# Performance work log

Hardware: AMD Instinct MI355X
Metric: run time of the kernel (lower is better)

## Reference

```python
import jax, jax.numpy as jnp
import numpy as np

B, S, DIM = 64, 576, 768
KEEP_TOKEN = 64  # module keeps KEEP_TOKEN-1 top patches + 1 pooled extra token
HID = 128       # autoencoder bottleneck


def setup_inputs() -> dict:
    key = jax.random.key(0)
    k1, k2, k3, k4 = jax.random.split(key, 4)
    cls_emb = jax.random.normal(k1, (B, DIM), dtype=jnp.float32)
    fm = jax.random.normal(k2, (B, S, DIM), dtype=jnp.float32)
    # autoencoder: Linear(dim,128) -> Tanh -> Linear(128,dim); y = x @ W + b
    W1 = jax.random.normal(k3, (DIM, HID), dtype=jnp.float32) / np.sqrt(DIM)
    b1 = jnp.zeros((HID,), dtype=jnp.float32)
    W2 = jax.random.normal(k4, (HID, DIM), dtype=jnp.float32) / np.sqrt(HID)
    b2 = jnp.zeros((DIM,), dtype=jnp.float32)
    return {"cls_emb": cls_emb, "fm": fm, "W1": W1, "b1": b1, "W2": W2, "b2": b2}


def reference(cls_emb, fm, W1, b1, W2, b2):
    # cls attention scores over patch tokens: [B, S]
    cls_attn = jnp.einsum('bd,bsd->bs', cls_emb, fm)
    # top-(K-1) patches by cls attention (largest, sorted)
    _, idx = jax.lax.top_k(cls_attn, KEEP_TOKEN - 1)           # [B, K-1]
    top_token = jnp.take_along_axis(fm, idx[:, :, None], axis=1)  # [B, K-1, DIM]
    # mask selected positions (one_hot(idx).sum(1) -> 0/1 since topk idx unique)
    batch_ix = jnp.arange(fm.shape[0])[:, None]
    one_hot_idx = jnp.zeros_like(cls_attn).at[batch_ix, idx].add(1.0)  # [B, S]
    weight = jax.nn.softmax(one_hot_idx * -10000.0 + cls_attn, axis=1)[:, :, None]
    extra_token = jnp.sum(weight * fm, axis=1, keepdims=True)  # [B, 1, DIM]
    visual_tokens = jnp.concatenate([top_token, extra_token], axis=1)  # [B, K, DIM]
    ae = lambda x: jnp.tanh(x @ W1 + b1) @ W2 + b2
    return ae(visual_tokens), ae(cls_emb)
```

## Files before the change

### kernel.cpp

```cpp
#include <hip/hip_runtime.h>
#include <math.h>

#define BB   64
#define SS   576
#define DD   768
#define KTOP 63
#define KEEP 64
#define HH   128
#define NROW (BB*KEEP + BB)
#define SCH  24

typedef unsigned long long ull;

__global__ __launch_bounds__(256) void k_scores(const float* __restrict__ cls,
                                                const float* __restrict__ fm,
                                                float* __restrict__ scores)
{
  int gw = (blockIdx.x * blockDim.x + threadIdx.x) >> 6;
  int lane = threadIdx.x & 63;
  if (gw >= BB * SS) return;
  int b = gw / SS, s = gw - b * SS;
  const float4* frow = (const float4*)(fm + ((size_t)b * SS + s) * DD);
  const float4* crow = (const float4*)(cls + (size_t)b * DD);
  double acc = 0.0;
#pragma unroll
  for (int j = 0; j < 3; ++j) {
    float4 f = frow[lane + 64 * j];
    float4 c = crow[lane + 64 * j];
    acc += (double)f.x * c.x + (double)f.y * c.y + (double)f.z * c.z + (double)f.w * c.w;
  }
#pragma unroll
  for (int off = 32; off > 0; off >>= 1) acc += __shfl_down(acc, off, 64);
  if (lane == 0) scores[(size_t)b * SS + s] = (float)acc;
}

__global__ __launch_bounds__(576) void k_rank(const float* __restrict__ scores,
                                              int* __restrict__ idxout,
                                              float* __restrict__ wprime)
{
  __shared__ ull keys[SS];
  __shared__ float redm[9], redz[9];
  int b = blockIdx.x, tid = threadIdx.x;
  int lane = tid & 63, wid = tid >> 6;
  float sc = scores[(size_t)b * SS + tid];
  unsigned int u = __float_as_uint(sc);
  u = (u & 0x80000000u) ? ~u : (u | 0x80000000u);
  ull key = ((ull)u << 32) | (ull)(0xFFFFFFFFu - (unsigned)tid);
  keys[tid] = key;
  __syncthreads();
  int rank = 0;
#pragma unroll 8
  for (int s = 0; s < SS; ++s) rank += (keys[s] > key) ? 1 : 0;
  bool sel = rank < KTOP;
  if (sel) idxout[b * KEEP + rank] = tid;
  float m = sel ? -1e30f : sc;
#pragma unroll
  for (int off = 32; off; off >>= 1) m = fmaxf(m, __shfl_xor(m, off, 64));
  if (lane == 0) redm[wid] = m;
  __syncthreads();
  float M = redm[0];
#pragma unroll
  for (int i = 1; i < 9; ++i) M = fmaxf(M, redm[i]);
  float e = sel ? 0.f : expf(sc - M);
  float z = e;
#pragma unroll
  for (int off = 32; off; off >>= 1) z += __shfl_xor(z, off, 64);
  if (lane == 0) redz[wid] = z;
  __syncthreads();
  float Z = redz[0];
#pragma unroll
  for (int i = 1; i < 9; ++i) Z += redz[i];
  wprime[(size_t)b * SS + tid] = e / Z;
}

__global__ __launch_bounds__(192) void k_extra2(const float* __restrict__ wprime,
                                                const float* __restrict__ fm,
                                                float* __restrict__ epart)
{
  int b = blockIdx.x, p = blockIdx.y, tid = threadIdx.x;
  const float* fbase = fm + ((size_t)b * SS + p * SCH) * DD + tid * 4;
  const float* wp = wprime + (size_t)b * SS + p * SCH;
  float4 acc = make_float4(0.f, 0.f, 0.f, 0.f);
#pragma unroll
  for (int r = 0; r < SCH; ++r) {
    float w = wp[r];
    float4 v = *(const float4*)(fbase + (size_t)r * DD);
    acc.x = fmaf(w, v.x, acc.x); acc.y = fmaf(w, v.y, acc.y);
    acc.z = fmaf(w, v.z, acc.z); acc.w = fmaf(w, v.w, acc.w);
  }
  *(float4*)(epart + ((size_t)(b * SCH + p) * DD) + tid * 4) = acc;
}

__global__ __launch_bounds__(256) void k_ered(const float* __restrict__ epart,
                                              float* __restrict__ extra)
{
  int i = blockIdx.x * 256 + threadIdx.x;
  int b = i / (DD / 4), c4 = i - b * (DD / 4);
  const float4* P = (const float4*)epart;
  float4 s = make_float4(0.f, 0.f, 0.f, 0.f);
#pragma unroll
  for (int p = 0; p < SCH; ++p) {
    float4 t = P[(size_t)(b * SCH + p) * (DD / 4) + c4];
    s.x += t.x; s.y += t.y; s.z += t.z; s.w += t.w;
  }
  ((float4*)extra)[i] = s;
}

template<int CPB>
__global__ __launch_bounds__(256, 3) void k_ae1(const float* __restrict__ fm,
                                                const float* __restrict__ cls,
                                                const float* __restrict__ extra,
                                                const int* __restrict__ idxin,
                                                const float* __restrict__ W1,
                                                float* __restrict__ partial)
{
  __shared__ float Xs[64][68];
  __shared__ float Ws[64][132];
  __shared__ const float* rowptr[64];
  int g = blockIdx.x;
  int tid = threadIdx.x;

  if (tid < 64) {
    const float* p;
    if (g < BB) {
      p = (tid < KTOP) ? fm + ((size_t)g * SS + idxin[g * KEEP + tid]) * DD
                       : extra + (size_t)g * DD;
    } else {
      p = cls + (size_t)tid * DD;
    }
    rowptr[tid] = p;
  }

  int ty = tid >> 5, tx = tid & 31;
  int r0 = ty * 8, c0 = tx * 4;
  float acc[8][4] = {};

  for (int cc = 0; cc < CPB; ++cc) {
    int kb = (blockIdx.y * CPB + cc) * 64;
    __syncthreads();
#pragma unroll
    for (int i = 0; i < 4; ++i) {
      int f4 = tid + 256 * i;
      int r = f4 >> 4, k4 = f4 & 15;
      *(float4*)&Xs[r][k4 * 4] = *(const float4*)(rowptr[r] + kb + k4 * 4);
    }
#pragma unroll
    for (int i = 0; i < 8; ++i) {
      int f4 = tid + 256 * i;
      int wr = f4 >> 5, c4 = f4 & 31;
      *(float4*)&Ws[wr][c4 * 4] =
          *(const float4*)(W1 + (size_t)(kb + wr) * HH + c4 * 4);
    }
    __syncthreads();
#pragma unroll
    for (int q = 0; q < 16; ++q) {
      float4 xv[8], wv[4];
#pragma unroll
      for (int i = 0; i < 8; ++i) xv[i] = *(const float4*)&Xs[r0 + i][q * 4];
#pragma unroll
      for (int j = 0; j < 4; ++j) wv[j] = *(const float4*)&Ws[q * 4 + j][c0];
#pragma unroll
      for (int i = 0; i < 8; ++i) {
        float x;
        x = xv[i].x;
        acc[i][0] = fmaf(x, wv[0].x, acc[i][0]); acc[i][1] = fmaf(x, wv[0].y, acc[i][1]);
        acc[i][2] = fmaf(x, wv[0].z, acc[i][2]); acc[i][3] = fmaf(x, wv[0].w, acc[i][3]);
        x = xv[i].y;
        acc[i][0] = fmaf(x, wv[1].x, acc[i][0]); acc[i][1] = fmaf(x, wv[1].y, acc[i][1]);
        acc[i][2] = fmaf(x, wv[1].z, acc[i][2]); acc[i][3] = fmaf(x, wv[1].w, acc[i][3]);
        x = xv[i].z;
        acc[i][0] = fmaf(x, wv[2].x, acc[i][0]); acc[i][1] = fmaf(x, wv[2].y, acc[i][1]);
        acc[i][2] = fmaf(x, wv[2].z, acc[i][2]); acc[i][3] = fmaf(x, wv[2].w, acc[i][3]);
        x = xv[i].w;
        acc[i][0] = fmaf(x, wv[3].x, acc[i][0]); acc[i][1] = fmaf(x, wv[3].y, acc[i][1]);
        acc[i][2] = fmaf(x, wv[3].z, acc[i][2]); acc[i][3] = fmaf(x, wv[3].w, acc[i][3]);
      }
    }
  }
  float* P = partial + (size_t)blockIdx.y * ((size_t)NROW * HH);
#pragma unroll
  for (int i = 0; i < 8; ++i) {
    float4 v = make_float4(acc[i][0], acc[i][1], acc[i][2], acc[i][3]);
    *(float4*)&P[(size_t)(g * 64 + r0 + i) * HH + c0] = v;
  }
}

template<int NP>
__global__ __launch_bounds__(256) void k_hred(const float* __restrict__ partial,
                                              const float* __restrict__ b1,
                                              float* __restrict__ H)
{
  int i4 = blockIdx.x * 256 + threadIdx.x;
  const float4* P = (const float4*)partial;
  float4 s = P[i4];
#pragma unroll
  for (int p = 1; p < NP; ++p) {
    float4 t = P[(size_t)p * (NROW * HH / 4) + i4];
    s.x += t.x; s.y += t.y; s.z += t.z; s.w += t.w;
  }
  float4 bv = ((const float4*)b1)[i4 & 31];
  s.x = tanhf(s.x + bv.x); s.y = tanhf(s.y + bv.y);
  s.z = tanhf(s.z + bv.z); s.w = tanhf(s.w + bv.w);
  ((float4*)H)[i4] = s;
}

__global__ __launch_bounds__(256, 2) void k_ae2(const float* __restrict__ H,
                                                const float* __restrict__ W2,
                                                const float* __restrict__ b2,
                                                float* __restrict__ out)
{
  __shared__ float Hs[64][132];
  __shared__ float Ws[128][68];
  int g = blockIdx.x;
  int cb = blockIdx.y;
  int tid = threadIdx.x;

#pragma unroll
  for (int i = 0; i < 8; ++i) {
    int f4 = tid + 256 * i;
    int r = f4 >> 5, c4 = f4 & 31;
    *(float4*)&Hs[r][c4 * 4] = *(const float4*)(H + (size_t)(g * 64 + r) * HH + c4 * 4);
  }
#pragma unroll
  for (int i = 0; i < 8; ++i) {
    int f4 = tid + 256 * i;
    int wr = f4 >> 4, c4 = f4 & 15;
    *(float4*)&Ws[wr][c4 * 4] =
        *(const float4*)(W2 + (size_t)wr * DD + cb * 64 + c4 * 4);
  }
  __syncthreads();

  int ty = tid >> 4, tx = tid & 15;
  int r0 = ty * 4, c0 = tx * 4;
  float acc[4][4] = {};
#pragma unroll 4
  for (int q = 0; q < 32; ++q) {
    float4 xv[4], wv[4];
#pragma unroll
    for (int i = 0; i < 4; ++i) xv[i] = *(const float4*)&Hs[r0 + i][q * 4];
#pragma unroll
    for (int j = 0; j < 4; ++j) wv[j] = *(const float4*)&Ws[q * 4 + j][c0];
#pragma unroll
    for (int i = 0; i < 4; ++i) {
      float x;
      x = xv[i].x;
      acc[i][0] = fmaf(x, wv[0].x, acc[i][0]); acc[i][1] = fmaf(x, wv[0].y, acc[i][1]);
      acc[i][2] = fmaf(x, wv[0].z, acc[i][2]); acc[i][3] = fmaf(x, wv[0].w, acc[i][3]);
      x = xv[i].y;
      acc[i][0] = fmaf(x, wv[1].x, acc[i][0]); acc[i][1] = fmaf(x, wv[1].y, acc[i][1]);
      acc[i][2] = fmaf(x, wv[1].z, acc[i][2]); acc[i][3] = fmaf(x, wv[1].w, acc[i][3]);
      x = xv[i].z;
      acc[i][0] = fmaf(x, wv[2].x, acc[i][0]); acc[i][1] = fmaf(x, wv[2].y, acc[i][1]);
      acc[i][2] = fmaf(x, wv[2].z, acc[i][2]); acc[i][3] = fmaf(x, wv[2].w, acc[i][3]);
      x = xv[i].w;
      acc[i][0] = fmaf(x, wv[3].x, acc[i][0]); acc[i][1] = fmaf(x, wv[3].y, acc[i][1]);
      acc[i][2] = fmaf(x, wv[3].z, acc[i][2]); acc[i][3] = fmaf(x, wv[3].w, acc[i][3]);
    }
  }
  float4 bv = *(const float4*)&b2[cb * 64 + c0];
#pragma unroll
  for (int i = 0; i < 4; ++i) {
    float4 y = make_float4(acc[i][0] + bv.x, acc[i][1] + bv.y,
                           acc[i][2] + bv.z, acc[i][3] + bv.w);
    *(float4*)&out[(size_t)(g * 64 + r0 + i) * DD + cb * 64 + c0] = y;
  }
}

extern "C" void kernel_launch(void* const* d_in, const int* in_sizes, int n_in,
                              void* d_out, int out_size, void* d_ws, size_t ws_size,
                              hipStream_t stream)
{
  const float* cls = (const float*)d_in[0];
  const float* fm  = (const float*)d_in[1];
  const float* W1  = (const float*)d_in[2];
  const float* b1  = (const float*)d_in[3];
  const float* W2  = (const float*)d_in[4];
  const float* b2  = (const float*)d_in[5];
  float* out = (float*)d_out;

  char* ws = (char*)d_ws;
  float* scores  = (float*)ws;
  int*   idx     = (int*)(ws + 147456);
  float* extra   = (float*)(ws + 163840);
  float* wprime  = (float*)(ws + 360448);
  float* epart   = (float*)(ws + 507904);
  float* partial = (float*)(ws + 5226496);
  const size_t PSLICE = (size_t)NROW * HH * 4;

  hipLaunchKernelGGL(k_scores, dim3((BB * SS) / 4), dim3(256), 0, stream, cls, fm, scores);
  hipLaunchKernelGGL(k_rank,   dim3(BB),            dim3(576), 0, stream, scores, idx, wprime);
  hipLaunchKernelGGL(k_extra2, dim3(BB, SCH),       dim3(192), 0, stream, wprime, fm, epart);
  hipLaunchKernelGGL(k_ered,   dim3(BB * DD / 1024), dim3(256), 0, stream, epart, extra);

  if (ws_size >= 5226496 + 13 * PSLICE) {
    float* H = (float*)(ws + 5226496 + 12 * PSLICE);
    hipLaunchKernelGGL(k_ae1<1>,  dim3(65, 12),      dim3(256), 0, stream,
                       fm, cls, extra, idx, W1, partial);
    hipLaunchKernelGGL(k_hred<12>, dim3(NROW * HH / 1024), dim3(256), 0, stream,
                       partial, b1, H);
    hipLaunchKernelGGL(k_ae2,     dim3(65, 12),      dim3(256), 0, stream, H, W2, b2, out);
  } else {
    float* H = (float*)(ws + 5226496 + PSLICE);
    hipLaunchKernelGGL(k_ae1<12>, dim3(65, 1),       dim3(256), 0, stream,
                       fm, cls, extra, idx, W1, partial);
    hipLaunchKernelGGL(k_hred<1>, dim3(NROW * HH / 1024), dim3(256), 0, stream,
                       partial, b1, H);
    hipLaunchKernelGGL(k_ae2,     dim3(65, 12),      dim3(256), 0, stream, H, W2, b2, out);
  }
}
```

Measured before the change: 99.23 us.

## Use packed fp16 dot2 for autoencoder GEMMs with fp16 hidden buffer

```diff
diff --git a/kernel.cpp b/kernel.cpp
--- a/kernel.cpp
+++ b/kernel.cpp
@@ -11,6 +11,21 @@
 #define SCH  24
 
 typedef unsigned long long ull;
+typedef _Float16 h2 __attribute__((ext_vector_type(2)));
+
+static __device__ __forceinline__ float DOT2(h2 a, h2 b, float c) {
+#if __has_builtin(__builtin_amdgcn_fdot2)
+  return __builtin_amdgcn_fdot2(a, b, c, false);
+#else
+  return fmaf((float)a[1], (float)b[1], fmaf((float)a[0], (float)b[0], c));
+#endif
+}
+static __device__ __forceinline__ unsigned PK(float x, float y) {
+  return __builtin_bit_cast(unsigned, __builtin_amdgcn_cvt_pkrtz(x, y));
+}
+static __device__ __forceinline__ h2 BC(unsigned u) {
+  return __builtin_bit_cast(h2, u);
+}
 
 __global__ __launch_bounds__(256) void k_scores(const float* __restrict__ cls,
                                                 const float* __restrict__ fm,
@@ -107,15 +122,15 @@
 }
 
 template<int CPB>
-__global__ __launch_bounds__(256, 3) void k_ae1(const float* __restrict__ fm,
-                                                const float* __restrict__ cls,
-                                                const float* __restrict__ extra,
-                                                const int* __restrict__ idxin,
-                                                const float* __restrict__ W1,
-                                                float* __restrict__ partial)
-{
-  __shared__ float Xs[64][68];
-  __shared__ float Ws[64][132];
+__global__ __launch_bounds__(128) void k_ae1(const float* __restrict__ fm,
+                                             const float* __restrict__ cls,
+                                             const float* __restrict__ extra,
+                                             const int* __restrict__ idxin,
+                                             const float* __restrict__ W1,
+                                             float* __restrict__ partial)
+{
+  __shared__ _Float16 Xs[64][68];
+  __shared__ unsigned Wp[32][132];
   __shared__ const float* rowptr[64];
   int g = blockIdx.x;
   int tid = threadIdx.x;
@@ -131,64 +146,70 @@
     rowptr[tid] = p;
   }
 
-  int ty = tid >> 5, tx = tid & 31;
-  int r0 = ty * 8, c0 = tx * 4;
-  float acc[8][4] = {};
+  int ty = tid >> 4, tx = tid & 15;
+  int r0 = ty * 8;
+  float acc[8][8] = {};
 
   for (int cc = 0; cc < CPB; ++cc) {
     int kb = (blockIdx.y * CPB + cc) * 64;
     __syncthreads();
 #pragma unroll
-    for (int i = 0; i < 4; ++i) {
-      int f4 = tid + 256 * i;
-      int r = f4 >> 4, k4 = f4 & 15;
-      *(float4*)&Xs[r][k4 * 4] = *(const float4*)(rowptr[r] + kb + k4 * 4);
-    }
-#pragma unroll
     for (int i = 0; i < 8; ++i) {
-      int f4 = tid + 256 * i;
-      int wr = f4 >> 5, c4 = f4 & 31;
-      *(float4*)&Ws[wr][c4 * 4] =
-          *(const float4*)(W1 + (size_t)(kb + wr) * HH + c4 * 4);
+      int id = tid + 128 * i;
+      int k4 = id & 15, r = id >> 4;
+      float4 v = *(const float4*)(rowptr[r] + kb + k4 * 4);
+      uint2 o = { PK(v.x, v.y), PK(v.z, v.w) };
+      *(uint2*)&Xs[r][k4 * 4] = o;
+    }
+#pragma unroll
+    for (int i = 0; i < 8; ++i) {
+      int id = tid + 128 * i;
+      int c4 = id & 31, kp = id >> 5;
+      const float* w0 = W1 + (size_t)(kb + 2 * kp) * HH + c4 * 4;
+      float4 a = *(const float4*)w0;
+      float4 b = *(const float4*)(w0 + HH);
+      uint4 o = { PK(a.x, b.x), PK(a.y, b.y), PK(a.z, b.z), PK(a.w, b.w) };
+      *(uint4*)&Wp[kp][c4 * 4] = o;
     }
     __syncthreads();
-#pragma unroll
+#pragma unroll 4
     for (int q = 0; q < 16; ++q) {
-      float4 xv[8], wv[4];
-#pragma unroll
-      for (int i = 0; i < 8; ++i) xv[i] = *(const float4*)&Xs[r0 + i][q * 4];
-#pragma unroll
-      for (int j = 0; j < 4; ++j) wv[j] = *(const float4*)&Ws[q * 4 + j][c0];
+      uint2 xr[8];
+#pragma unroll
+      for (int i = 0; i < 8; ++i) xr[i] = *(const uint2*)&Xs[r0 + i][q * 4];
+      uint4 wa0 = *(const uint4*)&Wp[2 * q][tx * 4];
+      uint4 wa1 = *(const uint4*)&Wp[2 * q][64 + tx * 4];
+      uint4 wb0 = *(const uint4*)&Wp[2 * q + 1][tx * 4];
+      uint4 wb1 = *(const uint4*)&Wp[2 * q + 1][64 + tx * 4];
 #pragma unroll
       for (int i = 0; i < 8; ++i) {
-        float x;
-        x = xv[i].x;
-        acc[i][0] = fmaf(x, wv[0].x, acc[i][0]); acc[i][1] = fmaf(x, wv[0].y, acc[i][1]);
-        acc[i][2] = fmaf(x, wv[0].z, acc[i][2]); acc[i][3] = fmaf(x, wv[0].w, acc[i][3]);
-        x = xv[i].y;
-        acc[i][0] = fmaf(x, wv[1].x, acc[i][0]); acc[i][1] = fmaf(x, wv[1].y, acc[i][1]);
-        acc[i][2] = fmaf(x, wv[1].z, acc[i][2]); acc[i][3] = fmaf(x, wv[1].w, acc[i][3]);
-        x = xv[i].z;
-        acc[i][0] = fmaf(x, wv[2].x, acc[i][0]); acc[i][1] = fmaf(x, wv[2].y, acc[i][1]);
-        acc[i][2] = fmaf(x, wv[2].z, acc[i][2]); acc[i][3] = fmaf(x, wv[2].w, acc[i][3]);
-        x = xv[i].w;
-        acc[i][0] = fmaf(x, wv[3].x, acc[i][0]); acc[i][1] = fmaf(x, wv[3].y, acc[i][1]);
-        acc[i][2] = fmaf(x, wv[3].z, acc[i][2]); acc[i][3] = fmaf(x, wv[3].w, acc[i][3]);
+        h2 a0 = BC(xr[i].x), a1 = BC(xr[i].y);
+        acc[i][0] = DOT2(a1, BC(wb0.x), DOT2(a0, BC(wa0.x), acc[i][0]));
+        acc[i][1] = DOT2(a1, BC(wb0.y), DOT2(a0, BC(wa0.y), acc[i][1]));
+        acc[i][2] = DOT2(a1, BC(wb0.z), DOT2(a0, BC(wa0.z), acc[i][2]));
+        acc[i][3] = DOT2(a1, BC(wb0.w), DOT2(a0, BC(wa0.w), acc[i][3]));
+        acc[i][4] = DOT2(a1, BC(wb1.x), DOT2(a0, BC(wa1.x), acc[i][4]));
+        acc[i][5] = DOT2(a1, BC(wb1.y), DOT2(a0, BC(wa1.y), acc[i][5]));
+        acc[i][6] = DOT2(a1, BC(wb1.z), DOT2(a0, BC(wa1.z), acc[i][6]));
+        acc[i][7] = DOT2(a1, BC(wb1.w), DOT2(a0, BC(wa1.w), acc[i][7]));
       }
     }
   }
-  float* P = partial + (size_t)blockIdx.y * ((size_t)NROW * HH);
+  float* P = partial + (size_t)(CPB == 1 ? blockIdx.y : 0) * ((size_t)NROW * HH);
 #pragma unroll
   for (int i = 0; i < 8; ++i) {
-    float4 v = make_float4(acc[i][0], acc[i][1], acc[i][2], acc[i][3]);
-    *(float4*)&P[(size_t)(g * 64 + r0 + i) * HH + c0] = v;
+    size_t row = (size_t)(g * 64 + r0 + i);
+    float4 v0 = make_float4(acc[i][0], acc[i][1], acc[i][2], acc[i][3]);
+    float4 v1 = make_float4(acc[i][4], acc[i][5], acc[i][6], acc[i][7]);
+    *(float4*)&P[row * HH + tx * 4] = v0;
+    *(float4*)&P[row * HH + 64 + tx * 4] = v1;
   }
 }
 
 template<int NP>
 __global__ __launch_bounds__(256) void k_hred(const float* __restrict__ partial,
                                               const float* __restrict__ b1,
-                                              float* __restrict__ H)
+                                              unsigned* __restrict__ H16)
 {
   int i4 = blockIdx.x * 256 + threadIdx.x;
   const float4* P = (const float4*)partial;
@@ -201,68 +222,74 @@
   float4 bv = ((const float4*)b1)[i4 & 31];
   s.x = tanhf(s.x + bv.x); s.y = tanhf(s.y + bv.y);
   s.z = tanhf(s.z + bv.z); s.w = tanhf(s.w + bv.w);
-  ((float4*)H)[i4] = s;
-}
-
-__global__ __launch_bounds__(256, 2) void k_ae2(const float* __restrict__ H,
-                                                const float* __restrict__ W2,
-                                                const float* __restrict__ b2,
-                                                float* __restrict__ out)
-{
-  __shared__ float Hs[64][132];
-  __shared__ float Ws[128][68];
-  int g = blockIdx.x;
-  int cb = blockIdx.y;
-  int tid = threadIdx.x;
-
-#pragma unroll
-  for (int i = 0; i < 8; ++i) {
-    int f4 = tid + 256 * i;
-    int r = f4 >> 5, c4 = f4 & 31;
-    *(float4*)&Hs[r][c4 * 4] = *(const float4*)(H + (size_t)(g * 64 + r) * HH + c4 * 4);
-  }
-#pragma unroll
-  for (int i = 0; i < 8; ++i) {
-    int f4 = tid + 256 * i;
-    int wr = f4 >> 4, c4 = f4 & 15;
-    *(float4*)&Ws[wr][c4 * 4] =
-        *(const float4*)(W2 + (size_t)wr * DD + cb * 64 + c4 * 4);
+  uint2 o = { PK(s.x, s.y), PK(s.z, s.w) };
+  ((uint2*)H16)[i4] = o;
+}
+
+__global__ __launch_bounds__(128) void k_ae2(const unsigned* __restrict__ H16,
+                                             const float* __restrict__ W2,
+                                             const float* __restrict__ b2,
+                                             float* __restrict__ out)
+{
+  __shared__ _Float16 Hs[64][132];
+  __shared__ unsigned Wp[64][132];
+  int g = blockIdx.x, cb = blockIdx.y, tid = threadIdx.x;
+
+#pragma unroll
+  for (int i = 0; i < 16; ++i) {
+    int id = tid + 128 * i;
+    int k4 = id & 31, r = id >> 5;
+    uint2 v = ((const uint2*)H16)[(size_t)(g * 64 + r) * (HH / 4) + k4];
+    *(uint2*)&Hs[r][k4 * 4] = v;
+  }
+#pragma unroll
+  for (int i = 0; i < 16; ++i) {
+    int id = tid + 128 * i;
+    int c4 = id & 31, kp = id >> 5;
+    const float* w0 = W2 + (size_t)(2 * kp) * DD + cb * 128 + c4 * 4;
+    float4 a = *(const float4*)w0;
+    float4 b = *(const float4*)(w0 + DD);
+    uint4 o = { PK(a.x, b.x), PK(a.y, b.y), PK(a.z, b.z), PK(a.w, b.w) };
+    *(uint4*)&Wp[kp][c4 * 4] = o;
   }
   __syncthreads();
 
   int ty = tid >> 4, tx = tid & 15;
-  int r0 = ty * 4, c0 = tx * 4;
-  float acc[4][4] = {};
+  int r0 = ty * 8;
+  float acc[8][8] = {};
 #pragma unroll 4
   for (int q = 0; q < 32; ++q) {
-    float4 xv[4], wv[4];
-#pragma unroll
-    for (int i = 0; i < 4; ++i) xv[i] = *(const float4*)&Hs[r0 + i][q * 4];
-#pragma unroll
-    for (int j = 0; j < 4; ++j) wv[j] = *(const float4*)&Ws[q * 4 + j][c0];
-#pragma unroll
-    for (int i = 0; i < 4; ++i) {
-      float x;
-      x = xv[i].x;
-      acc[i][0] = fmaf(x, wv[0].x, acc[i][0]); acc[i][1] = fmaf(x, wv[0].y, acc[i][1]);
-      acc[i][2] = fmaf(x, wv[0].z, acc[i][2]); acc[i][3] = fmaf(x, wv[0].w, acc[i][3]);
-      x = xv[i].y;
-      acc[i][0] = fmaf(x, wv[1].x, acc[i][0]); acc[i][1] = fmaf(x, wv[1].y, acc[i][1]);
-      acc[i][2] = fmaf(x, wv[1].z, acc[i][2]); acc[i][3] = fmaf(x, wv[1].w, acc[i][3]);
-      x = xv[i].z;
-      acc[i][0] = fmaf(x, wv[2].x, acc[i][0]); acc[i][1] = fmaf(x, wv[2].y, acc[i][1]);
-      acc[i][2] = fmaf(x, wv[2].z, acc[i][2]); acc[i][3] = fmaf(x, wv[2].w, acc[i][3]);
-      x = xv[i].w;
-      acc[i][0] = fmaf(x, wv[3].x, acc[i][0]); acc[i][1] = fmaf(x, wv[3].y, acc[i][1]);
-      acc[i][2] = fmaf(x, wv[3].z, acc[i][2]); acc[i][3] = fmaf(x, wv[3].w, acc[i][3]);
-    }
-  }
-  float4 bv = *(const float4*)&b2[cb * 64 + c0];
-#pragma unroll
-  for (int i = 0; i < 4; ++i) {
-    float4 y = make_float4(acc[i][0] + bv.x, acc[i][1] + bv.y,
-                           acc[i][2] + bv.z, acc[i][3] + bv.w);
-    *(float4*)&out[(size_t)(g * 64 + r0 + i) * DD + cb * 64 + c0] = y;
+    uint2 xr[8];
+#pragma unroll
+    for (int i = 0; i < 8; ++i) xr[i] = *(const uint2*)&Hs[r0 + i][q * 4];
+    uint4 wa0 = *(const uint4*)&Wp[2 * q][tx * 4];
+    uint4 wa1 = *(const uint4*)&Wp[2 * q][64 + tx * 4];
+    uint4 wb0 = *(const uint4*)&Wp[2 * q + 1][tx * 4];
+    uint4 wb1 = *(const uint4*)&Wp[2 * q + 1][64 + tx * 4];
+#pragma unroll
+    for (int i = 0; i < 8; ++i) {
+      h2 a0 = BC(xr[i].x), a1 = BC(xr[i].y);
+      acc[i][0] = DOT2(a1, BC(wb0.x), DOT2(a0, BC(wa0.x), acc[i][0]));
+      acc[i][1] = DOT2(a1, BC(wb0.y), DOT2(a0, BC(wa0.y), acc[i][1]));
+      acc[i][2] = DOT2(a1, BC(wb0.z), DOT2(a0, BC(wa0.z), acc[i][2]));
+      acc[i][3] = DOT2(a1, BC(wb0.w), DOT2(a0, BC(wa0.w), acc[i][3]));
+      acc[i][4] = DOT2(a1, BC(wb1.x), DOT2(a0, BC(wa1.x), acc[i][4]));
+      acc[i][5] = DOT2(a1, BC(wb1.y), DOT2(a0, BC(wa1.y), acc[i][5]));
+      acc[i][6] = DOT2(a1, BC(wb1.z), DOT2(a0, BC(wa1.z), acc[i][6]));
+      acc[i][7] = DOT2(a1, BC(wb1.w), DOT2(a0, BC(wa1.w), acc[i][7]));
+    }
+  }
+  float4 bv0 = *(const float4*)&b2[cb * 128 + tx * 4];
+  float4 bv1 = *(const float4*)&b2[cb * 128 + 64 + tx * 4];
+#pragma unroll
+  for (int i = 0; i < 8; ++i) {
+    size_t row = (size_t)(g * 64 + r0 + i);
+    float4 y0 = make_float4(acc[i][0] + bv0.x, acc[i][1] + bv0.y,
+                            acc[i][2] + bv0.z, acc[i][3] + bv0.w);
+    float4 y1 = make_float4(acc[i][4] + bv1.x, acc[i][5] + bv1.y,
+                            acc[i][6] + bv1.z, acc[i][7] + bv1.w);
+    *(float4*)&out[row * DD + cb * 128 + tx * 4] = y0;
+    *(float4*)&out[row * DD + cb * 128 + 64 + tx * 4] = y1;
   }
 }
 
@@ -286,25 +313,26 @@
   float* epart   = (float*)(ws + 507904);
   float* partial = (float*)(ws + 5226496);
   const size_t PSLICE = (size_t)NROW * HH * 4;
+  const size_t H16SZ  = (size_t)NROW * HH * 2;
 
   hipLaunchKernelGGL(k_scores, dim3((BB * SS) / 4), dim3(256), 0, stream, cls, fm, scores);
   hipLaunchKernelGGL(k_rank,   dim3(BB),            dim3(576), 0, stream, scores, idx, wprime);
   hipLaunchKernelGGL(k_extra2, dim3(BB, SCH),       dim3(192), 0, stream, wprime, fm, epart);
   hipLaunchKernelGGL(k_ered,   dim3(BB * DD / 1024), dim3(256), 0, stream, epart, extra);
 
-  if (ws_size >= 5226496 + 13 * PSLICE) {
-    float* H = (float*)(ws + 5226496 + 12 * PSLICE);
-    hipLaunchKernelGGL(k_ae1<1>,  dim3(65, 12),      dim3(256), 0, stream,
+  if (ws_size >= 5226496 + 12 * PSLICE + H16SZ) {
+    unsigned* H16 = (unsigned*)(ws + 5226496 + 12 * PSLICE);
+    hipLaunchKernelGGL(k_ae1<1>,  dim3(65, 12),      dim3(128), 0, stream,
                        fm, cls, extra, idx, W1, partial);
     hipLaunchKernelGGL(k_hred<12>, dim3(NROW * HH / 1024), dim3(256), 0, stream,
-                       partial, b1, H);
-    hipLaunchKernelGGL(k_ae2,     dim3(65, 12),      dim3(256), 0, stream, H, W2, b2, out);
+                       partial, b1, H16);
+    hipLaunchKernelGGL(k_ae2,     dim3(65, 6),       dim3(128), 0, stream, H16, W2, b2, out);
   } else {
-    float* H = (float*)(ws + 5226496 + PSLICE);
-    hipLaunchKernelGGL(k_ae1<12>, dim3(65, 1),       dim3(256), 0, stream,
+    unsigned* H16 = (unsigned*)(ws + 5226496 + PSLICE);
+    hipLaunchKernelGGL(k_ae1<12>, dim3(65, 1),       dim3(128), 0, stream,
                        fm, cls, extra, idx, W1, partial);
     hipLaunchKernelGGL(k_hred<1>, dim3(NROW * HH / 1024), dim3(256), 0, stream,
-                       partial, b1, H);
-    hipLaunchKernelGGL(k_ae2,     dim3(65, 12),      dim3(256), 0, stream, H, W2, b2, out);
-  }
-}
+                       partial, b1, H16);
+    hipLaunchKernelGGL(k_ae2,     dim3(65, 6),       dim3(128), 0, stream, H16, W2, b2, out);
+  }
+}
```

Measured after the change: 100.9 us. No clear change (+1.7%).

## Fuse pooled extra-token reduction into rank kernel with sparse weight compaction

Applied to the files above, without the earlier changes.

```diff
diff --git a/kernel.cpp b/kernel.cpp
--- a/kernel.cpp
+++ b/kernel.cpp
@@ -8,7 +8,6 @@
 #define KEEP 64
 #define HH   128
 #define NROW (BB*KEEP + BB)
-#define SCH  24
 
 typedef unsigned long long ull;
 
@@ -35,11 +34,16 @@
 }
 
 __global__ __launch_bounds__(576) void k_rank(const float* __restrict__ scores,
+                                              const float* __restrict__ fm,
                                               int* __restrict__ idxout,
-                                              float* __restrict__ wprime)
+                                              float* __restrict__ extra)
 {
   __shared__ ull keys[SS];
+  __shared__ int cis[SS];
+  __shared__ float cws[SS];
   __shared__ float redm[9], redz[9];
+  __shared__ unsigned wcnt[9];
+  __shared__ float4 red[2][192];
   int b = blockIdx.x, tid = threadIdx.x;
   int lane = tid & 63, wid = tid >> 6;
   float sc = scores[(size_t)b * SS + tid];
@@ -70,40 +74,41 @@
   float Z = redz[0];
 #pragma unroll
   for (int i = 1; i < 9; ++i) Z += redz[i];
-  wprime[(size_t)b * SS + tid] = e / Z;
-}
-
-__global__ __launch_bounds__(192) void k_extra2(const float* __restrict__ wprime,
-                                                const float* __restrict__ fm,
-                                                float* __restrict__ epart)
-{
-  int b = blockIdx.x, p = blockIdx.y, tid = threadIdx.x;
-  const float* fbase = fm + ((size_t)b * SS + p * SCH) * DD + tid * 4;
-  const float* wp = wprime + (size_t)b * SS + p * SCH;
-  float4 acc = make_float4(0.f, 0.f, 0.f, 0.f);
-#pragma unroll
-  for (int r = 0; r < SCH; ++r) {
-    float w = wp[r];
-    float4 v = *(const float4*)(fbase + (size_t)r * DD);
-    acc.x = fmaf(w, v.x, acc.x); acc.y = fmaf(w, v.y, acc.y);
-    acc.z = fmaf(w, v.z, acc.z); acc.w = fmaf(w, v.w, acc.w);
-  }
-  *(float4*)(epart + ((size_t)(b * SCH + p) * DD) + tid * 4) = acc;
-}
-
-__global__ __launch_bounds__(256) void k_ered(const float* __restrict__ epart,
-                                              float* __restrict__ extra)
-{
-  int i = blockIdx.x * 256 + threadIdx.x;
-  int b = i / (DD / 4), c4 = i - b * (DD / 4);
-  const float4* P = (const float4*)epart;
-  float4 s = make_float4(0.f, 0.f, 0.f, 0.f);
-#pragma unroll
-  for (int p = 0; p < SCH; ++p) {
-    float4 t = P[(size_t)(b * SCH + p) * (DD / 4) + c4];
-    s.x += t.x; s.y += t.y; s.z += t.z; s.w += t.w;
-  }
-  ((float4*)extra)[i] = s;
+  float w = e / Z;
+  bool keep = w > 1e-10f;
+  ull ball = __ballot(keep);
+  int wpre = __popcll(ball & ((1ull << lane) - 1ull));
+  if (lane == 0) wcnt[wid] = (unsigned)__popcll(ball);
+  __syncthreads();
+  int base = 0, n = 0;
+#pragma unroll
+  for (int i = 0; i < 9; ++i) {
+    base += (i < wid) ? (int)wcnt[i] : 0;
+    n += (int)wcnt[i];
+  }
+  if (keep) {
+    int pos = base + wpre;
+    cis[pos] = tid;
+    cws[pos] = w;
+  }
+  __syncthreads();
+  int sub = tid / 192, col = tid - sub * 192;
+  const float* fb = fm + (size_t)b * SS * DD + col * 4;
+  float4 a = make_float4(0.f, 0.f, 0.f, 0.f);
+  for (int r = sub; r < n; r += 3) {
+    float wv = cws[r];
+    float4 v = *(const float4*)(fb + (size_t)cis[r] * DD);
+    a.x = fmaf(wv, v.x, a.x); a.y = fmaf(wv, v.y, a.y);
+    a.z = fmaf(wv, v.z, a.z); a.w = fmaf(wv, v.w, a.w);
+  }
+  if (sub > 0) red[sub - 1][col] = a;
+  __syncthreads();
+  if (sub == 0) {
+    float4 t1 = red[0][col], t2 = red[1][col];
+    a.x += t1.x + t2.x; a.y += t1.y + t2.y;
+    a.z += t1.z + t2.z; a.w += t1.w + t2.w;
+    *(float4*)(extra + (size_t)b * DD + col * 4) = a;
+  }
 }
 
 template<int CPB>
@@ -177,7 +182,7 @@
       }
     }
   }
-  float* P = partial + (size_t)blockIdx.y * ((size_t)NROW * HH);
+  float* P = partial + (size_t)(CPB == 1 ? blockIdx.y : 0) * ((size_t)NROW * HH);
 #pragma unroll
   for (int i = 0; i < 8; ++i) {
     float4 v = make_float4(acc[i][0], acc[i][1], acc[i][2], acc[i][3]);
@@ -282,25 +287,22 @@
   float* scores  = (float*)ws;
   int*   idx     = (int*)(ws + 147456);
   float* extra   = (float*)(ws + 163840);
-  float* wprime  = (float*)(ws + 360448);
-  float* epart   = (float*)(ws + 507904);
-  float* partial = (float*)(ws + 5226496);
+  float* partial = (float*)(ws + 360448);
   const size_t PSLICE = (size_t)NROW * HH * 4;
 
   hipLaunchKernelGGL(k_scores, dim3((BB * SS) / 4), dim3(256), 0, stream, cls, fm, scores);
-  hipLaunchKernelGGL(k_rank,   dim3(BB),            dim3(576), 0, stream, scores, idx, wprime);
-  hipLaunchKernelGGL(k_extra2, dim3(BB, SCH),       dim3(192), 0, stream, wprime, fm, epart);
-  hipLaunchKernelGGL(k_ered,   dim3(BB * DD / 1024), dim3(256), 0, stream, epart, extra);
-
-  if (ws_size >= 5226496 + 13 * PSLICE) {
-    float* H = (float*)(ws + 5226496 + 12 * PSLICE);
+  hipLaunchKernelGGL(k_rank,   dim3(BB),            dim3(576), 0, stream,
+                     scores, fm, idx, extra);
+
+  if (ws_size >= 360448 + 13 * PSLICE) {
+    float* H = (float*)(ws + 360448 + 12 * PSLICE);
     hipLaunchKernelGGL(k_ae1<1>,  dim3(65, 12),      dim3(256), 0, stream,
                        fm, cls, extra, idx, W1, partial);
     hipLaunchKernelGGL(k_hred<12>, dim3(NROW * HH / 1024), dim3(256), 0, stream,
                        partial, b1, H);
     hipLaunchKernelGGL(k_ae2,     dim3(65, 12),      dim3(256), 0, stream, H, W2, b2, out);
   } else {
-    float* H = (float*)(ws + 5226496 + PSLICE);
+    float* H = (float*)(ws + 360448 + PSLICE);
     hipLaunchKernelGGL(k_ae1<12>, dim3(65, 1),       dim3(256), 0, stream,
                        fm, cls, extra, idx, W1, partial);
     hipLaunchKernelGGL(k_hred<1>, dim3(NROW * HH / 1024), dim3(256), 0, stream,
```

New measurement: 94.08 us. 1.05x faster.
